# Performance work log

Hardware: AMD Instinct MI355X
Metric: run time of the kernel (lower is better)

Reference implementation:

```python
import jax, jax.numpy as jnp
import numpy as np
from jax.ops import segment_sum, segment_max

N = 100000   # nodes
E = 1600000  # edges
B = 256      # graphs
H = 128      # hidden_channels
F_IN = 4     # input_size
EPS = 1e-5


def _graph_norm(x, w, b, ms, batch):
    # PyG GraphNorm: out = w * (x - ms*mean_g) / sqrt(var_g + eps) + b
    cnt = jnp.maximum(segment_sum(jnp.ones((x.shape[0],), x.dtype), batch, num_segments=B), 1.0)
    mean = segment_sum(x, batch, num_segments=B) / cnt[:, None]
    out = x - mean[batch] * ms
    var = segment_sum(out * out, batch, num_segments=B) / cnt[:, None]
    return w * out / jnp.sqrt(var + EPS)[batch] + b


def _gcn(x, W, b, src, dst):
    # GCNConv with self-loops and symmetric normalization (src/dst already include self-loops)
    h = x @ W                                              # [N, H]
    deg = segment_sum(jnp.ones_like(src, dtype=h.dtype), dst, num_segments=N)
    dinv = jax.lax.rsqrt(jnp.maximum(deg, 1.0))
    norm = dinv[src] * dinv[dst]                           # [E+N]
    return segment_sum(norm[:, None] * h[src], dst, num_segments=N) + b


def _seg_softmax(gate, batch):
    gmax = segment_max(gate, batch, num_segments=B)
    e = jnp.exp(gate - gmax[batch])
    den = segment_sum(e, batch, num_segments=B)
    return e / den[batch]


def setup_inputs() -> dict:
    key = jax.random.key(0)
    ks = jax.random.split(key, 16)
    x = jax.random.normal(ks[0], (N, F_IN), jnp.float32)
    edge_index = jax.random.randint(ks[1], (2, E), 0, N, dtype=jnp.int64)
    batch = jnp.sort(jax.random.randint(ks[2], (N,), 0, B, dtype=jnp.int64))
    r = lambda k, shp, fan: jax.random.normal(k, shp, jnp.float32) / np.sqrt(fan)
    inp = {
        "x": x, "edge_index": edge_index, "batch": batch,
        "W1": r(ks[3], (F_IN, H), F_IN), "b1": jnp.zeros((H,), jnp.float32),
        "W2": r(ks[4], (H, H), H), "b2": jnp.zeros((H,), jnp.float32),
        "W3": r(ks[5], (H, H), H), "b3": jnp.zeros((H,), jnp.float32),
        "gn0_w": jnp.ones((F_IN,), jnp.float32), "gn0_b": jnp.zeros((F_IN,), jnp.float32), "gn0_ms": jnp.ones((F_IN,), jnp.float32),
        "gn1_w": jnp.ones((H,), jnp.float32), "gn1_b": jnp.zeros((H,), jnp.float32), "gn1_ms": jnp.ones((H,), jnp.float32),
        "gn2_w": jnp.ones((H,), jnp.float32), "gn2_b": jnp.zeros((H,), jnp.float32), "gn2_ms": jnp.ones((H,), jnp.float32),
        "gn3_w": jnp.ones((H,), jnp.float32), "gn3_b": jnp.zeros((H,), jnp.float32), "gn3_ms": jnp.ones((H,), jnp.float32),
        "g1": r(ks[6], (H, H), H), "gb1": jnp.zeros((H,), jnp.float32),
        "g2": r(ks[7], (H, H), H), "gb2": jnp.zeros((H,), jnp.float32),
        "g3": r(ks[8], (H, 1), H), "gb3": jnp.zeros((1,), jnp.float32),
        "l1": r(ks[9], (H, H), H), "lb1": jnp.zeros((H,), jnp.float32),
        "l2": r(ks[10], (H, H), H), "lb2": jnp.zeros((H,), jnp.float32),
        "l3": r(ks[11], (H, 1), H), "lb3": jnp.zeros((1,), jnp.float32),
    }
    return inp


def reference(x, edge_index, batch, W1, b1, W2, b2, W3, b3,
              gn0_w, gn0_b, gn0_ms, gn1_w, gn1_b, gn1_ms,
              gn2_w, gn2_b, gn2_ms, gn3_w, gn3_b, gn3_ms,
              g1, gb1, g2, gb2, g3, gb3,
              l1, lb1, l2, lb2, l3, lb3):
    loop = jnp.arange(N, dtype=edge_index.dtype)
    src = jnp.concatenate([edge_index[0], loop])
    dst = jnp.concatenate([edge_index[1], loop])

    h = _graph_norm(x, gn0_w, gn0_b, gn0_ms, batch)
    h = _gcn(h, W1, b1, src, dst)
    h = jax.nn.relu(_graph_norm(h, gn1_w, gn1_b, gn1_ms, batch))
    h = _gcn(h, W2, b2, src, dst)
    h = jax.nn.relu(_graph_norm(h, gn2_w, gn2_b, gn2_ms, batch))
    h = _gcn(h, W3, b3, src, dst)
    h = _graph_norm(h, gn3_w, gn3_b, gn3_ms, batch)

    # GlobalAttention: gate_nn -> scalar gate per node, segment softmax, weighted sum
    g = jax.nn.relu(h @ g1 + gb1)
    g = jax.nn.relu(g @ g2 + gb2)
    gate = g @ g3 + gb3                                   # [N, 1]
    attn = _seg_softmax(gate, batch)                      # [N, 1]
    pooled = segment_sum(attn * h, batch, num_segments=B) # [B, H]

    o = jax.nn.relu(pooled @ l1 + lb1)
    o = jax.nn.relu(o @ l2 + lb2)
    return o @ l3 + lb3                                   # [B, 1]
```

## Files before the change

kernel.cpp:

```cpp
#include <hip/hip_runtime.h>
#include <hip/hip_bf16.h>

#define NN 100000
#define NE 1600000
#define NB 256
#define HD 128
#define EPS 1e-5f
#define NBUK 1563
#define SLOTB 1536
#define EPB 8192
#define NCHK 8

typedef __attribute__((ext_vector_type(8))) short bf16x8v;
typedef __attribute__((ext_vector_type(4))) float f32x4v;

__device__ __forceinline__ float rd_dyn(const void* p, int i, int fflag) {
    if (fflag) {
        unsigned short u = ((const unsigned short*)p)[i];
        return __uint_as_float(((unsigned)u) << 16);
    }
    return ((const float*)p)[i];
}

__device__ __forceinline__ int rd_idx(const int* p, int k, int iflag) {
    return iflag ? p[k] : p[2 * k];
}

__device__ __forceinline__ unsigned short f2bf(float v) {
    __hip_bfloat16 b = __float2bfloat16(v);
    return *(unsigned short*)&b;
}

__device__ __forceinline__ float bflo(unsigned u) { return __uint_as_float(u << 16); }
__device__ __forceinline__ float bfhi(unsigned u) { return __uint_as_float(u & 0xFFFF0000u); }
__device__ __forceinline__ unsigned packbf(float a, float b) {
    return (unsigned)f2bf(a) | ((unsigned)f2bf(b) << 16);
}

__global__ void k_mark7(unsigned short* __restrict__ out, int n) {
    int i = blockIdx.x * blockDim.x + threadIdx.x;
    if (i < n) out[i] = 0x40E0;
}

__global__ void k_detect(const int* __restrict__ batch, const unsigned* __restrict__ w,
                         int* __restrict__ flags, int n) {
    int i = blockIdx.x * blockDim.x + threadIdx.x;
    if (i == 0 && w[0] == 0x3F803F80u) atomicOr(&flags[1], 1);
    if (i < n && (i & 1) && batch[i] != 0) atomicOr(&flags[0], 1);
}

struct CvtArgs {
    const void* p[30];
    int n[30];
    int off[30];
    const void* wp[4];
};
__global__ void k_cvtf_all(CvtArgs a, float* __restrict__ out,
                           unsigned short* __restrict__ WT,
                           const int* __restrict__ fflagp) {
    int j = blockIdx.y;
    int i = blockIdx.x * blockDim.x + threadIdx.x;
    int ff = *fflagp;
    if (j < 30) {
        if (i >= a.n[j]) return;
        out[a.off[j] + i] = rd_dyn(a.p[j], i, ff);
    } else {
        int mat = j - 30;
        if (i >= 16384) return;
        int nidx = i >> 7, k = i & 127;
        WT[mat * 16384 + nidx * 128 + k] = f2bf(rd_dyn(a.wp[mat], k * 128 + nidx, ff));
    }
}

__global__ void k_start(const int* __restrict__ batch, const int* __restrict__ iflagp,
                        int* __restrict__ start, int* __restrict__ batch32,
                        int* __restrict__ bcur, int n) {
    int i = blockIdx.x * blockDim.x + threadIdx.x;
    if (i >= n) return;
    if (i < NBUK) bcur[i] = i * SLOTB;
    int ifl = *iflagp;
    int b = rd_idx(batch, i, ifl); b = b < 0 ? 0 : (b > NB - 1 ? NB - 1 : b);
    batch32[i] = b;
    int bp;
    if (i == 0) bp = -1;
    else { bp = rd_idx(batch, i - 1, ifl); bp = bp < 0 ? 0 : (bp > NB - 1 ? NB - 1 : bp); }
    for (int g = bp + 1; g <= b; ++g) start[g] = i;
    if (i == n - 1) { for (int g = b + 1; g <= NB; ++g) start[g] = n; }
}

__global__ __launch_bounds__(256) void k_bfill(const int* __restrict__ ei,
                                               const int* __restrict__ iflagp,
                                               int* __restrict__ bcur,
                                               unsigned* __restrict__ bkte, int e) {
    __shared__ int lh[NBUK];
    __shared__ int lbase[NBUK];
    int ifl = *iflagp;
    for (int b = threadIdx.x; b < NBUK; b += 256) lh[b] = 0;
    __syncthreads();
    int s0 = blockIdx.x * EPB;
    int s1 = s0 + EPB; if (s1 > e) s1 = e;
    for (int i = s0 + threadIdx.x; i < s1; i += 256) {
        int d = rd_idx(ei, NE + i, ifl);
        int s = rd_idx(ei, i, ifl);
        if ((unsigned)d < (unsigned)NN && (unsigned)s < (unsigned)NN)
            atomicAdd(&lh[d >> 6], 1);
    }
    __syncthreads();
    for (int b = threadIdx.x; b < NBUK; b += 256) {
        int c = lh[b];
        if (c) { lbase[b] = atomicAdd(&bcur[b], c); lh[b] = 0; }
    }
    __syncthreads();
    for (int i = s0 + threadIdx.x; i < s1; i += 256) {
        int d = rd_idx(ei, NE + i, ifl);
        int s = rd_idx(ei, i, ifl);
        if ((unsigned)d < (unsigned)NN && (unsigned)s < (unsigned)NN) {
            int b = d >> 6;
            int li = atomicAdd(&lh[b], 1);
            bkte[lbase[b] + li] = ((unsigned)s << 6) | (unsigned)(d & 63);
        }
    }
}

__global__ __launch_bounds__(256) void k_csrfin(const unsigned* __restrict__ bkte,
                                                const int* __restrict__ bcur,
                                                int* __restrict__ rowptr,
                                                int* __restrict__ cnt,
                                                float* __restrict__ dinv,
                                                int* __restrict__ esrc) {
    __shared__ int lc[64];
    __shared__ int lcur[64];
    int b = blockIdx.x, t = threadIdx.x;
    int base = b * 64;
    if (t < 64) lc[t] = 0;
    __syncthreads();
    int r0 = b * SLOTB, r1 = bcur[b];
    for (int j = r0 + t; j < r1; j += 256)
        atomicAdd(&lc[(int)(bkte[j] & 63u)], 1);
    __syncthreads();
    if (t < 64) {
        int v = lc[t];
        int inc = v;
#pragma unroll
        for (int off = 1; off < 64; off <<= 1) {
            int nv = __shfl_up(inc, off, 64);
            if (t >= off) inc += nv;
        }
        int ex = r0 + inc - v;
        lcur[t] = ex;
        int node = base + t;
        if (node < NN) {
            rowptr[node] = ex;
            cnt[node] = v;
            dinv[node] = rsqrtf((float)(v + 1));
        }
    }
    __syncthreads();
    for (int j = r0 + t; j < r1; j += 256) {
        unsigned p = bkte[j];
        int slot = atomicAdd(&lcur[p & 63u], 1);
        esrc[slot] = (int)(p >> 6);
    }
}

__global__ __launch_bounds__(256) void k_gn4(const void* __restrict__ x,
                                             const float* __restrict__ w,
                                             const float* __restrict__ bb,
                                             const float* __restrict__ ms,
                                             const int* __restrict__ start,
                                             const int* __restrict__ fflagp,
                                             float* __restrict__ out) {
    int g = blockIdx.x;
    int s0 = start[g], s1 = start[g + 1];
    if (s1 <= s0) return;
    int ff = *fflagp;
    float cnt = (float)(s1 - s0);
    int t = threadIdx.x;
    __shared__ float4 rs[256], rq[256];
    float sx = 0.f, sy = 0.f, sz = 0.f, sw = 0.f;
    float qx = 0.f, qy = 0.f, qz = 0.f, qw = 0.f;
    for (int n = s0 + t; n < s1; n += 256) {
        float4 v;
        if (ff) {
            uint2 u = ((const uint2*)x)[n];
            v.x = bflo(u.x); v.y = bfhi(u.x); v.z = bflo(u.y); v.w = bfhi(u.y);
        } else {
            v = ((const float4*)x)[n];
        }
        sx += v.x; sy += v.y; sz += v.z; sw += v.w;
        qx = fmaf(v.x, v.x, qx); qy = fmaf(v.y, v.y, qy);
        qz = fmaf(v.z, v.z, qz); qw = fmaf(v.w, v.w, qw);
    }
    rs[t] = make_float4(sx, sy, sz, sw);
    rq[t] = make_float4(qx, qy, qz, qw);
    __syncthreads();
    for (int off = 128; off; off >>= 1) {
        if (t < off) {
            rs[t].x += rs[t + off].x; rs[t].y += rs[t + off].y;
            rs[t].z += rs[t + off].z; rs[t].w += rs[t + off].w;
            rq[t].x += rq[t + off].x; rq[t].y += rq[t + off].y;
            rq[t].z += rq[t + off].z; rq[t].w += rq[t + off].w;
        }
        __syncthreads();
    }
    float4 S = rs[0], Q = rq[0];
    float4 wv = ((const float4*)w)[0];
    float4 bv = ((const float4*)bb)[0];
    float4 mv = ((const float4*)ms)[0];
    float4 mean = make_float4(S.x / cnt, S.y / cnt, S.z / cnt, S.w / cnt);
    float4 sub = make_float4(mean.x * mv.x, mean.y * mv.y, mean.z * mv.z, mean.w * mv.w);
    float4 scale;
    scale.x = wv.x * rsqrtf(Q.x / cnt - 2.f * sub.x * mean.x + sub.x * sub.x + EPS);
    scale.y = wv.y * rsqrtf(Q.y / cnt - 2.f * sub.y * mean.y + sub.y * sub.y + EPS);
    scale.z = wv.z * rsqrtf(Q.z / cnt - 2.f * sub.z * mean.z + sub.z * sub.z + EPS);
    scale.w = wv.w * rsqrtf(Q.w / cnt - 2.f * sub.w * mean.w + sub.w * sub.w + EPS);
    float4* op = (float4*)out;
    for (int n = s0 + t; n < s1; n += 256) {
        float4 v;
        if (ff) {
            uint2 u = ((const uint2*)x)[n];
            v.x = bflo(u.x); v.y = bfhi(u.x); v.z = bflo(u.y); v.w = bfhi(u.y);
        } else {
            v = ((const float4*)x)[n];
        }
        float4 o;
        o.x = scale.x * (v.x - sub.x) + bv.x;
        o.y = scale.y * (v.y - sub.y) + bv.y;
        o.z = scale.z * (v.z - sub.z) + bv.z;
        o.w = scale.w * (v.w - sub.w) + bv.w;
        op[n] = o;
    }
}

__global__ __launch_bounds__(256) void k_gnstats_part(const unsigned* __restrict__ Xu,
                                                      const int* __restrict__ start,
                                                      float* __restrict__ PS,
                                                      float* __restrict__ PQ) {
    int g = blockIdx.x, k = blockIdx.y;
    int s0 = start[g], s1 = start[g + 1];
    int len = (s1 - s0 + NCHK - 1) / NCHK;
    int c0 = s0 + k * len, c1 = c0 + len; if (c1 > s1) c1 = s1;
    int t = threadIdx.x;
    int cp = t & 63, p = t >> 6;
    __shared__ float r0s[256], r1s[256], r0q[256], r1q[256];
    float s0a = 0.f, s1a = 0.f, q0a = 0.f, q1a = 0.f;
    for (int n = c0 + p; n < c1; n += 4) {
        unsigned u = Xu[n * 64 + cp];
        float lo = bflo(u), hi = bfhi(u);
        s0a += lo; q0a = fmaf(lo, lo, q0a);
        s1a += hi; q1a = fmaf(hi, hi, q1a);
    }
    r0s[t] = s0a; r1s[t] = s1a; r0q[t] = q0a; r1q[t] = q1a;
    __syncthreads();
    if (p == 0) {
        float a0 = r0s[cp] + r0s[64 + cp] + r0s[128 + cp] + r0s[192 + cp];
        float a1 = r1s[cp] + r1s[64 + cp] + r1s[128 + cp] + r1s[192 + cp];
        float b0 = r0q[cp] + r0q[64 + cp] + r0q[128 + cp] + r0q[192 + cp];
        float b1 = r1q[cp] + r1q[64 + cp] + r1q[128 + cp] + r1q[192 + cp];
        int bidx = (g * NCHK + k) * 128;
        PS[bidx + 2 * cp] = a0; PS[bidx + 2 * cp + 1] = a1;
        PQ[bidx + 2 * cp] = b0; PQ[bidx + 2 * cp + 1] = b1;
    }
}

__global__ __launch_bounds__(128) void k_gnstats_final(const float* __restrict__ PS,
                                                       const float* __restrict__ PQ,
                                                       const float* __restrict__ w,
                                                       const float* __restrict__ ms,
                                                       const int* __restrict__ start,
                                                       float* __restrict__ SUB,
                                                       float* __restrict__ SCALE) {
    int g = blockIdx.x, c = threadIdx.x;
    int n = start[g + 1] - start[g];
    if (n <= 0) return;
    float cnt = (float)n;
    float s = 0.f, q = 0.f;
#pragma unroll
    for (int k = 0; k < NCHK; ++k) {
        s += PS[(g * NCHK + k) * 128 + c];
        q += PQ[(g * NCHK + k) * 128 + c];
    }
    float mean = s / cnt;
    float sq = q / cnt;
    float sub = mean * ms[c];
    float var = sq - 2.f * sub * mean + sub * sub;
    SUB[g * 128 + c] = sub;
    SCALE[g * 128 + c] = w[c] * rsqrtf(var + EPS);
}

__global__ __launch_bounds__(256) void k_gather4gemm(const int* __restrict__ rowptr,
                                                     const int* __restrict__ cnt,
                                                     const int* __restrict__ esrc,
                                                     const float* __restrict__ dinv,
                                                     const float* __restrict__ h0,
                                                     const float* __restrict__ W1,
                                                     const float* __restrict__ b1,
                                                     unsigned* __restrict__ Xu) {
    __shared__ float w1s[512];
    __shared__ float b1s[128];
    int tid = threadIdx.x;
    w1s[tid] = W1[tid];
    w1s[256 + tid] = W1[256 + tid];
    if (tid < 128) b1s[tid] = b1[tid];
    __syncthreads();
    int node = blockIdx.x * 4 + (tid >> 6);
    int lane = tid & 63;
    if (node >= NN) return;
    int r0 = rowptr[node], r1 = r0 + cnt[node];
    const float4* h4 = (const float4*)h0;
    float ax = 0.f, ay = 0.f, az = 0.f, aw = 0.f;
    for (int j = r0 + lane; j < r1; j += 64) {
        int s = esrc[j];
        float dv = dinv[s];
        float4 h = h4[s];
        ax = fmaf(dv, h.x, ax); ay = fmaf(dv, h.y, ay);
        az = fmaf(dv, h.z, az); aw = fmaf(dv, h.w, aw);
    }
#pragma unroll
    for (int mask = 1; mask <= 32; mask <<= 1) {
        ax += __shfl_xor(ax, mask, 64); ay += __shfl_xor(ay, mask, 64);
        az += __shfl_xor(az, mask, 64); aw += __shfl_xor(aw, mask, 64);
    }
    float dd = dinv[node];
    float4 hn = h4[node];
    float za = dd * ax + dd * dd * hn.x;
    float zb = dd * ay + dd * dd * hn.y;
    float zc = dd * az + dd * dd * hn.z;
    float zd = dd * aw + dd * dd * hn.w;
    int c0 = 2 * lane, c1 = 2 * lane + 1;
    float v0 = za * w1s[c0] + zb * w1s[128 + c0] + zc * w1s[256 + c0] + zd * w1s[384 + c0] + b1s[c0];
    float v1 = za * w1s[c1] + zb * w1s[128 + c1] + zc * w1s[256 + c1] + zd * w1s[384 + c1] + b1s[c1];
    Xu[node * 64 + lane] = packbf(v0, v1);
}

__global__ __launch_bounds__(256) void k_gemm_mfma_bf(const unsigned* __restrict__ Xu,
                                                      const int* __restrict__ batch32,
                                                      const float* __restrict__ SUB,
                                                      const float* __restrict__ SCALE,
                                                      const float* __restrict__ gnb,
                                                      int relu,
                                                      const unsigned short* __restrict__ WT,
                                                      const float* __restrict__ dinv,
                                                      unsigned short* __restrict__ out) {
    __shared__ unsigned short xs[16][136];
    int base = blockIdx.x * 16;
    int tid = threadIdx.x;
    for (int idx = tid; idx < 1024; idx += 256) {
        int r = idx >> 6, cp = idx & 63;
        int g = batch32[base + r];
        unsigned u = Xu[(base + r) * 64 + cp];
        float2 sub = ((const float2*)(SUB + g * 128))[cp];
        float2 sc  = ((const float2*)(SCALE + g * 128))[cp];
        float2 gb  = ((const float2*)gnb)[cp];
        float va = (bflo(u) - sub.x) * sc.x + gb.x;
        float vb = (bfhi(u) - sub.y) * sc.y + gb.y;
        if (relu) { va = fmaxf(va, 0.f); vb = fmaxf(vb, 0.f); }
        xs[r][2 * cp] = f2bf(va);
        xs[r][2 * cp + 1] = f2bf(vb);
    }
    __syncthreads();
    int wave = tid >> 6, lane = tid & 63;
    int m = lane & 15, quad = lane >> 4;
    f32x4v acc0 = {0.f, 0.f, 0.f, 0.f}, acc1 = {0.f, 0.f, 0.f, 0.f};
    int c0 = wave * 32 + m, c1 = c0 + 16;
#pragma unroll
    for (int kk = 0; kk < 4; ++kk) {
        int ko = kk * 32 + quad * 8;
        bf16x8v a  = *(const bf16x8v*)&xs[m][ko];
        bf16x8v b0 = *(const bf16x8v*)&WT[c0 * 128 + ko];
        bf16x8v b1 = *(const bf16x8v*)&WT[c1 * 128 + ko];
        acc0 = __builtin_amdgcn_mfma_f32_16x16x32_bf16(a, b0, acc0, 0, 0, 0);
        acc1 = __builtin_amdgcn_mfma_f32_16x16x32_bf16(a, b1, acc1, 0, 0, 0);
    }
#pragma unroll
    for (int reg = 0; reg < 4; ++reg) {
        int row = base + quad * 4 + reg;
        float dv = dinv[row];
        out[row * 128 + c0] = f2bf(dv * acc0[reg]);
        out[row * 128 + c1] = f2bf(dv * acc1[reg]);
    }
}

#define ACC4(u) do { \
    a0 += bflo((u).x); a1 += bfhi((u).x); \
    a2 += bflo((u).y); a3 += bfhi((u).y); \
    a4 += bflo((u).z); a5 += bfhi((u).z); \
    a6 += bflo((u).w); a7 += bfhi((u).w); } while (0)

__global__ __launch_bounds__(256) void k_gather_bf(const int* __restrict__ rowptr,
                                                   const int* __restrict__ cnt,
                                                   const int* __restrict__ esrc,
                                                   const float* __restrict__ dinv,
                                                   const unsigned* __restrict__ h,
                                                   const float* __restrict__ bias,
                                                   unsigned* __restrict__ Xu) {
    int node = blockIdx.x * 4 + (threadIdx.x >> 6);
    int lane = threadIdx.x & 63;
    if (node >= NN) return;
    int q = lane >> 4, s = lane & 15;
    int r0 = rowptr[node], r1 = r0 + cnt[node];
    const uint4* hp = (const uint4*)h;
    float a0 = 0.f, a1 = 0.f, a2 = 0.f, a3 = 0.f;
    float a4 = 0.f, a5 = 0.f, a6 = 0.f, a7 = 0.f;
    int j = r0 + q;
    for (; j + 12 < r1; j += 16) {
        int e0 = esrc[j], e1 = esrc[j + 4], e2 = esrc[j + 8], e3 = esrc[j + 12];
        uint4 u0 = hp[e0 * 16 + s];
        uint4 u1 = hp[e1 * 16 + s];
        uint4 u2 = hp[e2 * 16 + s];
        uint4 u3 = hp[e3 * 16 + s];
        ACC4(u0); ACC4(u1); ACC4(u2); ACC4(u3);
    }
    for (; j + 4 < r1; j += 8) {
        int e0 = esrc[j], e1 = esrc[j + 4];
        uint4 u0 = hp[e0 * 16 + s];
        uint4 u1 = hp[e1 * 16 + s];
        ACC4(u0); ACC4(u1);
    }
    for (; j < r1; j += 4) {
        int e0 = esrc[j];
        uint4 u0 = hp[e0 * 16 + s];
        ACC4(u0);
    }
    a0 += __shfl_xor(a0, 16, 64); a0 += __shfl_xor(a0, 32, 64);
    a1 += __shfl_xor(a1, 16, 64); a1 += __shfl_xor(a1, 32, 64);
    a2 += __shfl_xor(a2, 16, 64); a2 += __shfl_xor(a2, 32, 64);
    a3 += __shfl_xor(a3, 16, 64); a3 += __shfl_xor(a3, 32, 64);
    a4 += __shfl_xor(a4, 16, 64); a4 += __shfl_xor(a4, 32, 64);
    a5 += __shfl_xor(a5, 16, 64); a5 += __shfl_xor(a5, 32, 64);
    a6 += __shfl_xor(a6, 16, 64); a6 += __shfl_xor(a6, 32, 64);
    a7 += __shfl_xor(a7, 16, 64); a7 += __shfl_xor(a7, 32, 64);
    int cp = 4 * s + q;
    float ax = q == 0 ? a0 : q == 1 ? a2 : q == 2 ? a4 : a6;
    float ay = q == 0 ? a1 : q == 1 ? a3 : q == 2 ? a5 : a7;
    float dd = dinv[node];
    unsigned us = h[node * 64 + cp];
    float2 bb = ((const float2*)bias)[cp];
    float ox = dd * (ax + bflo(us)) + bb.x;
    float oy = dd * (ay + bfhi(us)) + bb.y;
    Xu[node * 64 + cp] = packbf(ox, oy);
}

__global__ __launch_bounds__(256) void k_gate_fused(const unsigned* __restrict__ Xu,
                                                    const int* __restrict__ batch32,
                                                    const float* __restrict__ SUB,
                                                    const float* __restrict__ SCALE,
                                                    const float* __restrict__ gnb,
                                                    const unsigned short* __restrict__ GT1,
                                                    const float* __restrict__ gb1,
                                                    const unsigned short* __restrict__ GT2,
                                                    const float* __restrict__ gb2,
                                                    const float* __restrict__ g3,
                                                    const float* __restrict__ gb3,
                                                    float* __restrict__ gate) {
    __shared__ unsigned short xs[16][136];
    __shared__ unsigned short t1[16][136];
    __shared__ float redw[64];
    int base = blockIdx.x * 16;
    int tid = threadIdx.x;
    for (int idx = tid; idx < 1024; idx += 256) {
        int r = idx >> 6, cp = idx & 63;
        int g = batch32[base + r];
        unsigned u = Xu[(base + r) * 64 + cp];
        float2 sub = ((const float2*)(SUB + g * 128))[cp];
        float2 sc  = ((const float2*)(SCALE + g * 128))[cp];
        float2 gb  = ((const float2*)gnb)[cp];
        xs[r][2 * cp] = f2bf((bflo(u) - sub.x) * sc.x + gb.x);
        xs[r][2 * cp + 1] = f2bf((bfhi(u) - sub.y) * sc.y + gb.y);
    }
    __syncthreads();
    int wave = tid >> 6, lane = tid & 63;
    int m = lane & 15, quad = lane >> 4;
    int c0 = wave * 32 + m, c1 = c0 + 16;
    f32x4v acc0 = {0.f, 0.f, 0.f, 0.f}, acc1 = {0.f, 0.f, 0.f, 0.f};
#pragma unroll
    for (int kk = 0; kk < 4; ++kk) {
        int ko = kk * 32 + quad * 8;
        bf16x8v a  = *(const bf16x8v*)&xs[m][ko];
        bf16x8v b0 = *(const bf16x8v*)&GT1[c0 * 128 + ko];
        bf16x8v b1 = *(const bf16x8v*)&GT1[c1 * 128 + ko];
        acc0 = __builtin_amdgcn_mfma_f32_16x16x32_bf16(a, b0, acc0, 0, 0, 0);
        acc1 = __builtin_amdgcn_mfma_f32_16x16x32_bf16(a, b1, acc1, 0, 0, 0);
    }
    float bj0 = gb1[c0], bj1 = gb1[c1];
#pragma unroll
    for (int reg = 0; reg < 4; ++reg) {
        int row = quad * 4 + reg;
        t1[row][c0] = f2bf(fmaxf(acc0[reg] + bj0, 0.f));
        t1[row][c1] = f2bf(fmaxf(acc1[reg] + bj1, 0.f));
    }
    __syncthreads();
    f32x4v d0 = {0.f, 0.f, 0.f, 0.f}, d1 = {0.f, 0.f, 0.f, 0.f};
#pragma unroll
    for (int kk = 0; kk < 4; ++kk) {
        int ko = kk * 32 + quad * 8;
        bf16x8v a  = *(const bf16x8v*)&t1[m][ko];
        bf16x8v b0 = *(const bf16x8v*)&GT2[c0 * 128 + ko];
        bf16x8v b1 = *(const bf16x8v*)&GT2[c1 * 128 + ko];
        d0 = __builtin_amdgcn_mfma_f32_16x16x32_bf16(a, b0, d0, 0, 0, 0);
        d1 = __builtin_amdgcn_mfma_f32_16x16x32_bf16(a, b1, d1, 0, 0, 0);
    }
    float g30 = g3[c0], g31 = g3[c1];
    float bk0 = gb2[c0], bk1 = gb2[c1];
    float contrib[4];
#pragma unroll
    for (int reg = 0; reg < 4; ++reg) {
        float v0 = fmaxf(d0[reg] + bk0, 0.f);
        float v1 = fmaxf(d1[reg] + bk1, 0.f);
        contrib[reg] = v0 * g30 + v1 * g31;
    }
#pragma unroll
    for (int mask = 1; mask <= 8; mask <<= 1) {
#pragma unroll
        for (int reg = 0; reg < 4; ++reg)
            contrib[reg] += __shfl_xor(contrib[reg], mask, 64);
    }
    if (m == 0) {
#pragma unroll
        for (int reg = 0; reg < 4; ++reg)
            redw[wave * 16 + quad * 4 + reg] = contrib[reg];
    }
    __syncthreads();
    if (tid < 16) {
        float s = redw[tid] + redw[16 + tid] + redw[32 + tid] + redw[48 + tid];
        gate[base + tid] = s + gb3[0];
    }
}

__global__ __launch_bounds__(256) void k_smpool(const unsigned* __restrict__ Xu,
                                                const float* __restrict__ SUB,
                                                const float* __restrict__ SCALE,
                                                const float* __restrict__ gnb,
                                                const float* __restrict__ gate,
                                                const int* __restrict__ start,
                                                float* __restrict__ PP) {
    int g = blockIdx.x, kk = blockIdx.y;
    int s0 = start[g], s1 = start[g + 1];
    int t = threadIdx.x;
    __shared__ float red[256];
    __shared__ float r0s[256], r1s[256];
    if (s1 <= s0) {
        if (t < 64) {
            int bidx = (g * NCHK + kk) * 128;
            ((float2*)(PP + bidx))[t] = make_float2(0.f, 0.f);
        }
        return;
    }
    float m = -1e30f;
    for (int i = s0 + t; i < s1; i += 256) m = fmaxf(m, gate[i]);
    red[t] = m; __syncthreads();
    for (int off = 128; off; off >>= 1) { if (t < off) red[t] = fmaxf(red[t], red[t + off]); __syncthreads(); }
    m = red[0]; __syncthreads();
    float sden = 0.f;
    for (int i = s0 + t; i < s1; i += 256) sden += expf(gate[i] - m);
    red[t] = sden; __syncthreads();
    for (int off = 128; off; off >>= 1) { if (t < off) red[t] += red[t + off]; __syncthreads(); }
    float invden = 1.f / red[0];
    int len = (s1 - s0 + NCHK - 1) / NCHK;
    int c0 = s0 + kk * len, c1 = c0 + len; if (c1 > s1) c1 = s1;
    int cp = t & 63, p = t >> 6;
    float2 sub = ((const float2*)(SUB + g * 128))[cp];
    float2 sc  = ((const float2*)(SCALE + g * 128))[cp];
    float2 gb  = ((const float2*)gnb)[cp];
    float sa = 0.f, sb = 0.f;
    for (int n = c0 + p; n < c1; n += 4) {
        float a = expf(gate[n] - m) * invden;
        unsigned u = Xu[n * 64 + cp];
        sa += a * ((bflo(u) - sub.x) * sc.x + gb.x);
        sb += a * ((bfhi(u) - sub.y) * sc.y + gb.y);
    }
    r0s[t] = sa; r1s[t] = sb; __syncthreads();
    if (p == 0) {
        int bidx = (g * NCHK + kk) * 128;
        float2 o;
        o.x = r0s[cp] + r0s[64 + cp] + r0s[128 + cp] + r0s[192 + cp];
        o.y = r1s[cp] + r1s[64 + cp] + r1s[128 + cp] + r1s[192 + cp];
        ((float2*)(PP + bidx))[cp] = o;
    }
}

__global__ __launch_bounds__(128) void k_head(const float* __restrict__ PP,
                                              const float* __restrict__ l1, const float* __restrict__ lb1,
                                              const float* __restrict__ l2, const float* __restrict__ lb2,
                                              const float* __restrict__ l3, const float* __restrict__ lb3,
                                              const int* __restrict__ fflagp,
                                              void* __restrict__ out) {
    int g = blockIdx.x, t = threadIdx.x;
    __shared__ float p[128], o[128], red[128];
    float s = 0.f;
#pragma unroll
    for (int k = 0; k < NCHK; ++k) s += PP[(g * NCHK + k) * 128 + t];
    p[t] = s; __syncthreads();
    float a = 0.f;
    for (int k = 0; k < 128; ++k) a += p[k] * l1[k * 128 + t];
    a = fmaxf(a + lb1[t], 0.f);
    o[t] = a; __syncthreads();
    float b = 0.f;
    for (int k = 0; k < 128; ++k) b += o[k] * l2[k * 128 + t];
    b = fmaxf(b + lb2[t], 0.f);
    red[t] = b * l3[t]; __syncthreads();
    for (int off = 64; off; off >>= 1) { if (t < off) red[t] += red[t + off]; __syncthreads(); }
    if (t == 0) {
        float r = red[0] + lb3[0];
        if (*fflagp) ((__hip_bfloat16*)out)[g] = __float2bfloat16(r);
        else ((float*)out)[g] = r;
    }
}

extern "C" void kernel_launch(void* const* d_in, const int* in_sizes, int n_in,
                              void* d_out, int out_size, void* d_ws, size_t ws_size,
                              hipStream_t stream) {
    const void* x = d_in[0];
    const int* ei_raw = (const int*)d_in[1];
    const int* batch_raw = (const int*)d_in[2];
    (void)n_in; (void)out_size;

    char* ws = (char*)d_ws;
    size_t off = 0;
    auto alloc = [&](size_t bytes) -> void* {
        void* p = ws + off;
        off += (bytes + 255) & ~(size_t)255;
        return p;
    };
    unsigned* Xu  = (unsigned*)alloc((size_t)NN * HD * 2);
    float* Y      = (float*)alloc((size_t)NN * HD * 4);
    float* h0     = (float*)alloc((size_t)NN * 4 * 4);
    float* dinv   = (float*)alloc((size_t)NN * 4);
    float* gate   = (float*)alloc((size_t)NN * 4);
    int*   start  = (int*)alloc((size_t)(NB + 1) * 4);
    int*   batch32= (int*)alloc((size_t)NN * 4);
    float* P      = (float*)alloc((size_t)131072 * 4);
    unsigned short* WT = (unsigned short*)alloc((size_t)4 * 16384 * 2);
    float* SUB    = (float*)alloc((size_t)NB * HD * 4);
    float* SCALE  = (float*)alloc((size_t)NB * HD * 4);
    float* PS     = (float*)alloc((size_t)NB * NCHK * 128 * 4);
    float* PQ     = (float*)alloc((size_t)NB * NCHK * 128 * 4);
    int*   flags  = (int*)alloc(256);
    int*   rowptr = (int*)alloc((size_t)NN * 4);
    int*   cnt    = (int*)alloc((size_t)NN * 4);
    int*   esrc   = (int*)alloc((size_t)NBUK * SLOTB * 4);
    int*   bcur   = (int*)alloc((size_t)NBUK * 4);
    unsigned* bkte = (unsigned*)(Y + (size_t)NN * HD / 2);
    float* PP = PS;

    if (ws_size < off) {
        k_mark7<<<1, 256, 0, stream>>>((unsigned short*)d_out, NB);
        return;
    }

    int* iflag = flags;
    int* fflag = flags + 1;
    hipMemsetAsync(flags, 0, 8, stream);
    k_detect<<<(NN + 255) / 256, 256, 0, stream>>>(batch_raw, (const unsigned*)d_in[12], flags, NN);

    CvtArgs ca;
    float* fp[33];
    int maxn = 16384;
    {
        int poff = 0;
        for (int i = 3; i < 33; ++i) {
            int n = in_sizes[i];
            ca.p[i - 3] = d_in[i];
            ca.n[i - 3] = n;
            ca.off[i - 3] = poff;
            fp[i] = P + poff;
            poff += n;
            if (n > maxn) maxn = n;
        }
        ca.wp[0] = d_in[5];
        ca.wp[1] = d_in[7];
        ca.wp[2] = d_in[21];
        ca.wp[3] = d_in[23];
    }
    {
        dim3 grid((maxn + 255) / 256, 34);
        k_cvtf_all<<<grid, 256, 0, stream>>>(ca, P, WT, fflag);
    }
    const float *W1 = fp[3], *b1 = fp[4], *b2 = fp[6], *b3 = fp[8];
    const float *gn0w = fp[9],  *gn0b = fp[10], *gn0m = fp[11];
    const float *gn1w = fp[12], *gn1b = fp[13], *gn1m = fp[14];
    const float *gn2w = fp[15], *gn2b = fp[16], *gn2m = fp[17];
    const float *gn3w = fp[18], *gn3b = fp[19], *gn3m = fp[20];
    const float *gb1 = fp[22], *gb2 = fp[24], *g3 = fp[25], *gb3 = fp[26];
    const float *l1 = fp[27], *lb1 = fp[28], *l2 = fp[29], *lb2 = fp[30], *l3 = fp[31], *lb3 = fp[32];

    const unsigned short* WT2 = WT;
    const unsigned short* WT3 = WT + 16384;
    const unsigned short* GT1 = WT + 2 * 16384;
    const unsigned short* GT2 = WT + 3 * 16384;

    k_start<<<(NN + 255) / 256, 256, 0, stream>>>(batch_raw, iflag, start, batch32, bcur, NN);

    int ebg = (NE + EPB - 1) / EPB;
    k_bfill<<<ebg, 256, 0, stream>>>(ei_raw, iflag, bcur, bkte, NE);
    k_csrfin<<<NBUK, 256, 0, stream>>>(bkte, bcur, rowptr, cnt, dinv, esrc);

    k_gn4<<<NB, 256, 0, stream>>>(x, gn0w, gn0b, gn0m, start, fflag, h0);

    k_gather4gemm<<<(NN + 3) / 4, 256, 0, stream>>>(rowptr, cnt, esrc, dinv, h0, W1, b1, Xu);

    unsigned short* Yb = (unsigned short*)Y;
    dim3 sgrid(NB, NCHK);

    k_gnstats_part<<<sgrid, 256, 0, stream>>>(Xu, start, PS, PQ);
    k_gnstats_final<<<NB, 128, 0, stream>>>(PS, PQ, gn1w, gn1m, start, SUB, SCALE);
    k_gemm_mfma_bf<<<NN / 16, 256, 0, stream>>>(Xu, batch32, SUB, SCALE, gn1b, 1, WT2, dinv, Yb);
    k_gather_bf<<<(NN + 3) / 4, 256, 0, stream>>>(rowptr, cnt, esrc, dinv, (const unsigned*)Yb, b2, Xu);

    k_gnstats_part<<<sgrid, 256, 0, stream>>>(Xu, start, PS, PQ);
    k_gnstats_final<<<NB, 128, 0, stream>>>(PS, PQ, gn2w, gn2m, start, SUB, SCALE);
    k_gemm_mfma_bf<<<NN / 16, 256, 0, stream>>>(Xu, batch32, SUB, SCALE, gn2b, 1, WT3, dinv, Yb);
    k_gather_bf<<<(NN + 3) / 4, 256, 0, stream>>>(rowptr, cnt, esrc, dinv, (const unsigned*)Yb, b3, Xu);

    k_gnstats_part<<<sgrid, 256, 0, stream>>>(Xu, start, PS, PQ);
    k_gnstats_final<<<NB, 128, 0, stream>>>(PS, PQ, gn3w, gn3m, start, SUB, SCALE);
    k_gate_fused<<<NN / 16, 256, 0, stream>>>(Xu, batch32, SUB, SCALE, gn3b,
                                              GT1, gb1, GT2, gb2, g3, gb3, gate);
    k_smpool<<<sgrid, 256, 0, stream>>>(Xu, SUB, SCALE, gn3b, gate, start, PP);
    k_head<<<NB, 128, 0, stream>>>(PP, l1, lb1, l2, lb2, l3, lb3, fflag, d_out);
}
```

Measured before the change: 532.7 us.

## Fuse prep, CSR finalize with GraphNorm0, stats and pooling-head kernels

Merges k_start into the conversion kernel and k_csrfin with the first GraphNorm in one launch. Replaces the two-stage GraphNorm stats (partials plus final) with a single kernel per graph and channel segment. Merges softmax pooling with the MLP head, caching attention weights in shared memory. It also changes the first gather to spread channels across lanes. The aim is fewer launches and intermediate buffers, at the cost of less parallelism per graph in the stats and pooling kernels (256 or 1024 blocks instead of 2048).

```diff
diff --git a/kernel.cpp b/kernel.cpp
--- a/kernel.cpp
+++ b/kernel.cpp
@@ -9,7 +9,7 @@
 #define NBUK 1563
 #define SLOTB 1536
 #define EPB 8192
-#define NCHK 8
+#define MAXG 768
 
 typedef __attribute__((ext_vector_type(8))) short bf16x8v;
 typedef __attribute__((ext_vector_type(4))) float f32x4v;
@@ -55,37 +55,34 @@
     int off[30];
     const void* wp[4];
 };
-__global__ void k_cvtf_all(CvtArgs a, float* __restrict__ out,
-                           unsigned short* __restrict__ WT,
-                           const int* __restrict__ fflagp) {
+__global__ void k_prep(CvtArgs a, float* __restrict__ out,
+                       unsigned short* __restrict__ WT,
+                       const int* __restrict__ flagsp,
+                       const int* __restrict__ batch,
+                       int* __restrict__ start, int* __restrict__ batch32,
+                       int* __restrict__ bcur) {
     int j = blockIdx.y;
     int i = blockIdx.x * blockDim.x + threadIdx.x;
-    int ff = *fflagp;
     if (j < 30) {
         if (i >= a.n[j]) return;
-        out[a.off[j] + i] = rd_dyn(a.p[j], i, ff);
-    } else {
+        out[a.off[j] + i] = rd_dyn(a.p[j], i, flagsp[1]);
+    } else if (j < 34) {
         int mat = j - 30;
         if (i >= 16384) return;
         int nidx = i >> 7, k = i & 127;
-        WT[mat * 16384 + nidx * 128 + k] = f2bf(rd_dyn(a.wp[mat], k * 128 + nidx, ff));
-    }
-}
-
-__global__ void k_start(const int* __restrict__ batch, const int* __restrict__ iflagp,
-                        int* __restrict__ start, int* __restrict__ batch32,
-                        int* __restrict__ bcur, int n) {
-    int i = blockIdx.x * blockDim.x + threadIdx.x;
-    if (i >= n) return;
-    if (i < NBUK) bcur[i] = i * SLOTB;
-    int ifl = *iflagp;
-    int b = rd_idx(batch, i, ifl); b = b < 0 ? 0 : (b > NB - 1 ? NB - 1 : b);
-    batch32[i] = b;
-    int bp;
-    if (i == 0) bp = -1;
-    else { bp = rd_idx(batch, i - 1, ifl); bp = bp < 0 ? 0 : (bp > NB - 1 ? NB - 1 : bp); }
-    for (int g = bp + 1; g <= b; ++g) start[g] = i;
-    if (i == n - 1) { for (int g = b + 1; g <= NB; ++g) start[g] = n; }
+        WT[mat * 16384 + nidx * 128 + k] = f2bf(rd_dyn(a.wp[mat], k * 128 + nidx, flagsp[1]));
+    } else {
+        if (i >= NN) return;
+        if (i < NBUK) bcur[i] = i * SLOTB;
+        int ifl = flagsp[0];
+        int b = rd_idx(batch, i, ifl); b = b < 0 ? 0 : (b > NB - 1 ? NB - 1 : b);
+        batch32[i] = b;
+        int bp;
+        if (i == 0) bp = -1;
+        else { bp = rd_idx(batch, i - 1, ifl); bp = bp < 0 ? 0 : (bp > NB - 1 ? NB - 1 : bp); }
+        for (int g = bp + 1; g <= b; ++g) start[g] = i;
+        if (i == NN - 1) { for (int g = b + 1; g <= NB; ++g) start[g] = NN; }
+    }
 }
 
 __global__ __launch_bounds__(256) void k_bfill(const int* __restrict__ ei,
@@ -122,61 +119,62 @@
     }
 }
 
-__global__ __launch_bounds__(256) void k_csrfin(const unsigned* __restrict__ bkte,
-                                                const int* __restrict__ bcur,
-                                                int* __restrict__ rowptr,
-                                                int* __restrict__ cnt,
-                                                float* __restrict__ dinv,
-                                                int* __restrict__ esrc) {
-    __shared__ int lc[64];
-    __shared__ int lcur[64];
-    int b = blockIdx.x, t = threadIdx.x;
-    int base = b * 64;
-    if (t < 64) lc[t] = 0;
-    __syncthreads();
-    int r0 = b * SLOTB, r1 = bcur[b];
-    for (int j = r0 + t; j < r1; j += 256)
-        atomicAdd(&lc[(int)(bkte[j] & 63u)], 1);
-    __syncthreads();
-    if (t < 64) {
-        int v = lc[t];
-        int inc = v;
-#pragma unroll
-        for (int off = 1; off < 64; off <<= 1) {
-            int nv = __shfl_up(inc, off, 64);
-            if (t >= off) inc += nv;
-        }
-        int ex = r0 + inc - v;
-        lcur[t] = ex;
-        int node = base + t;
-        if (node < NN) {
-            rowptr[node] = ex;
-            cnt[node] = v;
-            dinv[node] = rsqrtf((float)(v + 1));
-        }
-    }
-    __syncthreads();
-    for (int j = r0 + t; j < r1; j += 256) {
-        unsigned p = bkte[j];
-        int slot = atomicAdd(&lcur[p & 63u], 1);
-        esrc[slot] = (int)(p >> 6);
-    }
-}
-
-__global__ __launch_bounds__(256) void k_gn4(const void* __restrict__ x,
-                                             const float* __restrict__ w,
-                                             const float* __restrict__ bb,
-                                             const float* __restrict__ ms,
-                                             const int* __restrict__ start,
-                                             const int* __restrict__ fflagp,
-                                             float* __restrict__ out) {
-    int g = blockIdx.x;
+__global__ __launch_bounds__(256) void k_csrfin_gn4(const unsigned* __restrict__ bkte,
+                                                    const int* __restrict__ bcur,
+                                                    int* __restrict__ rowptr,
+                                                    int* __restrict__ cnt,
+                                                    float* __restrict__ dinv,
+                                                    int* __restrict__ esrc,
+                                                    const void* __restrict__ x,
+                                                    const float* __restrict__ w,
+                                                    const float* __restrict__ bb,
+                                                    const float* __restrict__ ms,
+                                                    const int* __restrict__ start,
+                                                    const int* __restrict__ fflagp,
+                                                    float* __restrict__ out) {
+    int t = threadIdx.x;
+    if (blockIdx.x < NBUK) {
+        __shared__ int lc[64];
+        __shared__ int lcur[64];
+        int b = blockIdx.x;
+        int base = b * 64;
+        if (t < 64) lc[t] = 0;
+        __syncthreads();
+        int r0 = b * SLOTB, r1 = bcur[b];
+        for (int j = r0 + t; j < r1; j += 256)
+            atomicAdd(&lc[(int)(bkte[j] & 63u)], 1);
+        __syncthreads();
+        if (t < 64) {
+            int v = lc[t];
+            int inc = v;
+#pragma unroll
+            for (int off = 1; off < 64; off <<= 1) {
+                int nv = __shfl_up(inc, off, 64);
+                if (t >= off) inc += nv;
+            }
+            int ex = r0 + inc - v;
+            lcur[t] = ex;
+            int node = base + t;
+            if (node < NN) {
+                rowptr[node] = ex;
+                cnt[node] = v;
+                dinv[node] = rsqrtf((float)(v + 1));
+            }
+        }
+        __syncthreads();
+        for (int j = r0 + t; j < r1; j += 256) {
+            unsigned p = bkte[j];
+            int slot = atomicAdd(&lcur[p & 63u], 1);
+            esrc[slot] = (int)(p >> 6);
+        }
+        return;
+    }
+    __shared__ float4 rs[256], rq[256];
+    int g = blockIdx.x - NBUK;
     int s0 = start[g], s1 = start[g + 1];
     if (s1 <= s0) return;
     int ff = *fflagp;
-    float cnt = (float)(s1 - s0);
-    int t = threadIdx.x;
-    __shared__ float4 rs[256], rq[256];
+    float cntf = (float)(s1 - s0);
     float sx = 0.f, sy = 0.f, sz = 0.f, sw = 0.f;
     float qx = 0.f, qy = 0.f, qz = 0.f, qw = 0.f;
     for (int n = s0 + t; n < s1; n += 256) {
@@ -207,13 +205,13 @@
     float4 wv = ((const float4*)w)[0];
     float4 bv = ((const float4*)bb)[0];
     float4 mv = ((const float4*)ms)[0];
-    float4 mean = make_float4(S.x / cnt, S.y / cnt, S.z / cnt, S.w / cnt);
+    float4 mean = make_float4(S.x / cntf, S.y / cntf, S.z / cntf, S.w / cntf);
     float4 sub = make_float4(mean.x * mv.x, mean.y * mv.y, mean.z * mv.z, mean.w * mv.w);
     float4 scale;
-    scale.x = wv.x * rsqrtf(Q.x / cnt - 2.f * sub.x * mean.x + sub.x * sub.x + EPS);
-    scale.y = wv.y * rsqrtf(Q.y / cnt - 2.f * sub.y * mean.y + sub.y * sub.y + EPS);
-    scale.z = wv.z * rsqrtf(Q.z / cnt - 2.f * sub.z * mean.z + sub.z * sub.z + EPS);
-    scale.w = wv.w * rsqrtf(Q.w / cnt - 2.f * sub.w * mean.w + sub.w * sub.w + EPS);
+    scale.x = wv.x * rsqrtf(Q.x / cntf - 2.f * sub.x * mean.x + sub.x * sub.x + EPS);
+    scale.y = wv.y * rsqrtf(Q.y / cntf - 2.f * sub.y * mean.y + sub.y * sub.y + EPS);
+    scale.z = wv.z * rsqrtf(Q.z / cntf - 2.f * sub.z * mean.z + sub.z * sub.z + EPS);
+    scale.w = wv.w * rsqrtf(Q.w / cntf - 2.f * sub.w * mean.w + sub.w * sub.w + EPS);
     float4* op = (float4*)out;
     for (int n = s0 + t; n < s1; n += 256) {
         float4 v;
@@ -232,60 +230,47 @@
     }
 }
 
-__global__ __launch_bounds__(256) void k_gnstats_part(const unsigned* __restrict__ Xu,
-                                                      const int* __restrict__ start,
-                                                      float* __restrict__ PS,
-                                                      float* __restrict__ PQ) {
-    int g = blockIdx.x, k = blockIdx.y;
+__global__ __launch_bounds__(256) void k_gnstats1(const unsigned* __restrict__ Xu,
+                                                  const float* __restrict__ w,
+                                                  const float* __restrict__ ms,
+                                                  const int* __restrict__ start,
+                                                  float* __restrict__ SUB,
+                                                  float* __restrict__ SCALE) {
+    int g = blockIdx.x, seg = blockIdx.y;
     int s0 = start[g], s1 = start[g + 1];
-    int len = (s1 - s0 + NCHK - 1) / NCHK;
-    int c0 = s0 + k * len, c1 = c0 + len; if (c1 > s1) c1 = s1;
+    if (s1 <= s0) return;
     int t = threadIdx.x;
-    int cp = t & 63, p = t >> 6;
-    __shared__ float r0s[256], r1s[256], r0q[256], r1q[256];
-    float s0a = 0.f, s1a = 0.f, q0a = 0.f, q1a = 0.f;
-    for (int n = c0 + p; n < c1; n += 4) {
-        unsigned u = Xu[n * 64 + cp];
+    int wrd = t & 15;
+    int p = t >> 4;
+    int wbase = seg * 16 + wrd;
+    __shared__ float rs0[256], rs1[256], rq0[256], rq1[256];
+    float sa = 0.f, sb = 0.f, qa = 0.f, qb = 0.f;
+    for (int n = s0 + p; n < s1; n += 16) {
+        unsigned u = Xu[(size_t)n * 64 + wbase];
         float lo = bflo(u), hi = bfhi(u);
-        s0a += lo; q0a = fmaf(lo, lo, q0a);
-        s1a += hi; q1a = fmaf(hi, hi, q1a);
-    }
-    r0s[t] = s0a; r1s[t] = s1a; r0q[t] = q0a; r1q[t] = q1a;
-    __syncthreads();
-    if (p == 0) {
-        float a0 = r0s[cp] + r0s[64 + cp] + r0s[128 + cp] + r0s[192 + cp];
-        float a1 = r1s[cp] + r1s[64 + cp] + r1s[128 + cp] + r1s[192 + cp];
-        float b0 = r0q[cp] + r0q[64 + cp] + r0q[128 + cp] + r0q[192 + cp];
-        float b1 = r1q[cp] + r1q[64 + cp] + r1q[128 + cp] + r1q[192 + cp];
-        int bidx = (g * NCHK + k) * 128;
-        PS[bidx + 2 * cp] = a0; PS[bidx + 2 * cp + 1] = a1;
-        PQ[bidx + 2 * cp] = b0; PQ[bidx + 2 * cp + 1] = b1;
-    }
-}
-
-__global__ __launch_bounds__(128) void k_gnstats_final(const float* __restrict__ PS,
-                                                       const float* __restrict__ PQ,
-                                                       const float* __restrict__ w,
-                                                       const float* __restrict__ ms,
-                                                       const int* __restrict__ start,
-                                                       float* __restrict__ SUB,
-                                                       float* __restrict__ SCALE) {
-    int g = blockIdx.x, c = threadIdx.x;
-    int n = start[g + 1] - start[g];
-    if (n <= 0) return;
-    float cnt = (float)n;
-    float s = 0.f, q = 0.f;
-#pragma unroll
-    for (int k = 0; k < NCHK; ++k) {
-        s += PS[(g * NCHK + k) * 128 + c];
-        q += PQ[(g * NCHK + k) * 128 + c];
-    }
-    float mean = s / cnt;
-    float sq = q / cnt;
-    float sub = mean * ms[c];
-    float var = sq - 2.f * sub * mean + sub * sub;
-    SUB[g * 128 + c] = sub;
-    SCALE[g * 128 + c] = w[c] * rsqrtf(var + EPS);
+        sa += lo; qa = fmaf(lo, lo, qa);
+        sb += hi; qb = fmaf(hi, hi, qb);
+    }
+    rs0[t] = sa; rs1[t] = sb; rq0[t] = qa; rq1[t] = qb;
+    __syncthreads();
+    for (int off = 128; off >= 16; off >>= 1) {
+        if (t < off) {
+            rs0[t] += rs0[t + off]; rs1[t] += rs1[t + off];
+            rq0[t] += rq0[t + off]; rq1[t] += rq1[t + off];
+        }
+        __syncthreads();
+    }
+    if (t < 16) {
+        float cnt = (float)(s1 - s0);
+        int c0 = 2 * (seg * 16 + t), c1 = c0 + 1;
+        float mean0 = rs0[t] / cnt, mean1 = rs1[t] / cnt;
+        float sub0 = mean0 * ms[c0], sub1 = mean1 * ms[c1];
+        float var0 = rq0[t] / cnt - 2.f * sub0 * mean0 + sub0 * sub0;
+        float var1 = rq1[t] / cnt - 2.f * sub1 * mean1 + sub1 * sub1;
+        SUB[g * 128 + c0] = sub0; SUB[g * 128 + c1] = sub1;
+        SCALE[g * 128 + c0] = w[c0] * rsqrtf(var0 + EPS);
+        SCALE[g * 128 + c1] = w[c1] * rsqrtf(var1 + EPS);
+    }
 }
 
 __global__ __launch_bounds__(256) void k_gather4gemm(const int* __restrict__ rowptr,
@@ -306,27 +291,20 @@
     int node = blockIdx.x * 4 + (tid >> 6);
     int lane = tid & 63;
     if (node >= NN) return;
+    int ch = lane & 3;
     int r0 = rowptr[node], r1 = r0 + cnt[node];
-    const float4* h4 = (const float4*)h0;
-    float ax = 0.f, ay = 0.f, az = 0.f, aw = 0.f;
-    for (int j = r0 + lane; j < r1; j += 64) {
+    float acc = 0.f;
+    for (int j = r0 + (lane >> 2); j < r1; j += 16) {
         int s = esrc[j];
-        float dv = dinv[s];
-        float4 h = h4[s];
-        ax = fmaf(dv, h.x, ax); ay = fmaf(dv, h.y, ay);
-        az = fmaf(dv, h.z, az); aw = fmaf(dv, h.w, aw);
-    }
-#pragma unroll
-    for (int mask = 1; mask <= 32; mask <<= 1) {
-        ax += __shfl_xor(ax, mask, 64); ay += __shfl_xor(ay, mask, 64);
-        az += __shfl_xor(az, mask, 64); aw += __shfl_xor(aw, mask, 64);
-    }
+        acc = fmaf(dinv[s], h0[s * 4 + ch], acc);
+    }
+#pragma unroll
+    for (int mask = 4; mask <= 32; mask <<= 1)
+        acc += __shfl_xor(acc, mask, 64);
     float dd = dinv[node];
-    float4 hn = h4[node];
-    float za = dd * ax + dd * dd * hn.x;
-    float zb = dd * ay + dd * dd * hn.y;
-    float zc = dd * az + dd * dd * hn.z;
-    float zd = dd * aw + dd * dd * hn.w;
+    float z = dd * acc + dd * dd * h0[node * 4 + ch];
+    float za = __shfl(z, 0, 64), zb = __shfl(z, 1, 64);
+    float zc = __shfl(z, 2, 64), zd = __shfl(z, 3, 64);
     int c0 = 2 * lane, c1 = 2 * lane + 1;
     float v0 = za * w1s[c0] + zb * w1s[128 + c0] + zc * w1s[256 + c0] + zd * w1s[384 + c0] + b1s[c0];
     float v1 = za * w1s[c1] + zb * w1s[128 + c1] + zc * w1s[256 + c1] + zd * w1s[384 + c1] + b1s[c1];
@@ -527,78 +505,86 @@
     }
 }
 
-__global__ __launch_bounds__(256) void k_smpool(const unsigned* __restrict__ Xu,
-                                                const float* __restrict__ SUB,
-                                                const float* __restrict__ SCALE,
-                                                const float* __restrict__ gnb,
-                                                const float* __restrict__ gate,
-                                                const int* __restrict__ start,
-                                                float* __restrict__ PP) {
-    int g = blockIdx.x, kk = blockIdx.y;
+__global__ __launch_bounds__(256) void k_smpool_head(const unsigned* __restrict__ Xu,
+                                                     const float* __restrict__ SUB,
+                                                     const float* __restrict__ SCALE,
+                                                     const float* __restrict__ gnb,
+                                                     const float* __restrict__ gate,
+                                                     const int* __restrict__ start,
+                                                     const float* __restrict__ l1, const float* __restrict__ lb1,
+                                                     const float* __restrict__ l2, const float* __restrict__ lb2,
+                                                     const float* __restrict__ l3, const float* __restrict__ lb3,
+                                                     const int* __restrict__ fflagp,
+                                                     void* __restrict__ out) {
+    int g = blockIdx.x, t = threadIdx.x;
+    __shared__ float red[256];
+    __shared__ float att[MAXG];
+    __shared__ float4 rs4[256];
+    __shared__ float pool[128];
+    __shared__ float o[128];
     int s0 = start[g], s1 = start[g + 1];
-    int t = threadIdx.x;
-    __shared__ float red[256];
-    __shared__ float r0s[256], r1s[256];
-    if (s1 <= s0) {
-        if (t < 64) {
-            int bidx = (g * NCHK + kk) * 128;
-            ((float2*)(PP + bidx))[t] = make_float2(0.f, 0.f);
-        }
-        return;
-    }
+    int len = s1 - s0;
+    bool fits = len <= MAXG;
     float m = -1e30f;
     for (int i = s0 + t; i < s1; i += 256) m = fmaxf(m, gate[i]);
     red[t] = m; __syncthreads();
     for (int off = 128; off; off >>= 1) { if (t < off) red[t] = fmaxf(red[t], red[t + off]); __syncthreads(); }
     m = red[0]; __syncthreads();
     float sden = 0.f;
-    for (int i = s0 + t; i < s1; i += 256) sden += expf(gate[i] - m);
+    for (int i = s0 + t; i < s1; i += 256) {
+        float e = expf(gate[i] - m);
+        if (fits) att[i - s0] = e;
+        sden += e;
+    }
     red[t] = sden; __syncthreads();
     for (int off = 128; off; off >>= 1) { if (t < off) red[t] += red[t + off]; __syncthreads(); }
-    float invden = 1.f / red[0];
-    int len = (s1 - s0 + NCHK - 1) / NCHK;
-    int c0 = s0 + kk * len, c1 = c0 + len; if (c1 > s1) c1 = s1;
-    int cp = t & 63, p = t >> 6;
-    float2 sub = ((const float2*)(SUB + g * 128))[cp];
-    float2 sc  = ((const float2*)(SCALE + g * 128))[cp];
-    float2 gb  = ((const float2*)gnb)[cp];
-    float sa = 0.f, sb = 0.f;
-    for (int n = c0 + p; n < c1; n += 4) {
-        float a = expf(gate[n] - m) * invden;
-        unsigned u = Xu[n * 64 + cp];
-        sa += a * ((bflo(u) - sub.x) * sc.x + gb.x);
-        sb += a * ((bfhi(u) - sub.y) * sc.y + gb.y);
-    }
-    r0s[t] = sa; r1s[t] = sb; __syncthreads();
-    if (p == 0) {
-        int bidx = (g * NCHK + kk) * 128;
-        float2 o;
-        o.x = r0s[cp] + r0s[64 + cp] + r0s[128 + cp] + r0s[192 + cp];
-        o.y = r1s[cp] + r1s[64 + cp] + r1s[128 + cp] + r1s[192 + cp];
-        ((float2*)(PP + bidx))[cp] = o;
-    }
-}
-
-__global__ __launch_bounds__(128) void k_head(const float* __restrict__ PP,
-                                              const float* __restrict__ l1, const float* __restrict__ lb1,
-                                              const float* __restrict__ l2, const float* __restrict__ lb2,
-                                              const float* __restrict__ l3, const float* __restrict__ lb3,
-                                              const int* __restrict__ fflagp,
-                                              void* __restrict__ out) {
-    int g = blockIdx.x, t = threadIdx.x;
-    __shared__ float p[128], o[128], red[128];
-    float s = 0.f;
-#pragma unroll
-    for (int k = 0; k < NCHK; ++k) s += PP[(g * NCHK + k) * 128 + t];
-    p[t] = s; __syncthreads();
-    float a = 0.f;
-    for (int k = 0; k < 128; ++k) a += p[k] * l1[k * 128 + t];
-    a = fmaxf(a + lb1[t], 0.f);
-    o[t] = a; __syncthreads();
-    float b = 0.f;
-    for (int k = 0; k < 128; ++k) b += o[k] * l2[k * 128 + t];
-    b = fmaxf(b + lb2[t], 0.f);
-    red[t] = b * l3[t]; __syncthreads();
+    float invden = len > 0 ? 1.f / red[0] : 0.f;
+    __syncthreads();
+    int cp2 = t & 31, p = t >> 5;
+    float4 sb4 = {0.f, 0.f, 0.f, 0.f}, sc4 = {0.f, 0.f, 0.f, 0.f}, gb4 = {0.f, 0.f, 0.f, 0.f};
+    if (len > 0) {
+        sb4 = ((const float4*)(SUB + g * 128))[cp2];
+        sc4 = ((const float4*)(SCALE + g * 128))[cp2];
+        gb4 = ((const float4*)gnb)[cp2];
+    }
+    float a0 = 0.f, a1 = 0.f, a2 = 0.f, a3 = 0.f;
+    for (int n = s0 + p; n < s1; n += 8) {
+        float a = (fits ? att[n - s0] : expf(gate[n] - m)) * invden;
+        uint2 u = ((const uint2*)(Xu + (size_t)n * 64))[cp2];
+        a0 += a * ((bflo(u.x) - sb4.x) * sc4.x + gb4.x);
+        a1 += a * ((bfhi(u.x) - sb4.y) * sc4.y + gb4.y);
+        a2 += a * ((bflo(u.y) - sb4.z) * sc4.z + gb4.z);
+        a3 += a * ((bfhi(u.y) - sb4.w) * sc4.w + gb4.w);
+    }
+    rs4[t] = make_float4(a0, a1, a2, a3);
+    __syncthreads();
+    for (int off = 128; off >= 32; off >>= 1) {
+        if (t < off) {
+            rs4[t].x += rs4[t + off].x; rs4[t].y += rs4[t + off].y;
+            rs4[t].z += rs4[t + off].z; rs4[t].w += rs4[t + off].w;
+        }
+        __syncthreads();
+    }
+    if (t < 32) {
+        pool[4 * t]     = rs4[t].x;
+        pool[4 * t + 1] = rs4[t].y;
+        pool[4 * t + 2] = rs4[t].z;
+        pool[4 * t + 3] = rs4[t].w;
+    }
+    __syncthreads();
+    if (t < 128) {
+        float a = 0.f;
+        for (int k = 0; k < 128; ++k) a += pool[k] * l1[k * 128 + t];
+        o[t] = fmaxf(a + lb1[t], 0.f);
+    }
+    __syncthreads();
+    if (t < 128) {
+        float b = 0.f;
+        for (int k = 0; k < 128; ++k) b += o[k] * l2[k * 128 + t];
+        b = fmaxf(b + lb2[t], 0.f);
+        red[t] = b * l3[t];
+    }
+    __syncthreads();
     for (int off = 64; off; off >>= 1) { if (t < off) red[t] += red[t + off]; __syncthreads(); }
     if (t == 0) {
         float r = red[0] + lb3[0];
@@ -633,15 +619,12 @@
     unsigned short* WT = (unsigned short*)alloc((size_t)4 * 16384 * 2);
     float* SUB    = (float*)alloc((size_t)NB * HD * 4);
     float* SCALE  = (float*)alloc((size_t)NB * HD * 4);
-    float* PS     = (float*)alloc((size_t)NB * NCHK * 128 * 4);
-    float* PQ     = (float*)alloc((size_t)NB * NCHK * 128 * 4);
     int*   flags  = (int*)alloc(256);
     int*   rowptr = (int*)alloc((size_t)NN * 4);
     int*   cnt    = (int*)alloc((size_t)NN * 4);
     int*   esrc   = (int*)alloc((size_t)NBUK * SLOTB * 4);
     int*   bcur   = (int*)alloc((size_t)NBUK * 4);
     unsigned* bkte = (unsigned*)(Y + (size_t)NN * HD / 2);
-    float* PP = PS;
 
     if (ws_size < off) {
         k_mark7<<<1, 256, 0, stream>>>((unsigned short*)d_out, NB);
@@ -655,7 +638,6 @@
 
     CvtArgs ca;
     float* fp[33];
-    int maxn = 16384;
     {
         int poff = 0;
         for (int i = 3; i < 33; ++i) {
@@ -665,7 +647,6 @@
             ca.off[i - 3] = poff;
             fp[i] = P + poff;
             poff += n;
-            if (n > maxn) maxn = n;
         }
         ca.wp[0] = d_in[5];
         ca.wp[1] = d_in[7];
@@ -673,12 +654,12 @@
         ca.wp[3] = d_in[23];
     }
     {
-        dim3 grid((maxn + 255) / 256, 34);
-        k_cvtf_all<<<grid, 256, 0, stream>>>(ca, P, WT, fflag);
+        dim3 grid((NN + 255) / 256, 35);
+        k_prep<<<grid, 256, 0, stream>>>(ca, P, WT, flags, batch_raw, start, batch32, bcur);
     }
     const float *W1 = fp[3], *b1 = fp[4], *b2 = fp[6], *b3 = fp[8];
     const float *gn0w = fp[9],  *gn0b = fp[10], *gn0m = fp[11];
-    const float *gn1w = fp[12], *gn1b = fp[13], *gn1m = fp[14];
+    const float *gn1w = fp[12], *gn1m = fp[14], *gn1b = fp[13];
     const float *gn2w = fp[15], *gn2b = fp[16], *gn2m = fp[17];
     const float *gn3w = fp[18], *gn3b = fp[19], *gn3m = fp[20];
     const float *gb1 = fp[22], *gb2 = fp[24], *g3 = fp[25], *gb3 = fp[26];
@@ -689,33 +670,27 @@
     const unsigned short* GT1 = WT + 2 * 16384;
     const unsigned short* GT2 = WT + 3 * 16384;
 
-    k_start<<<(NN + 255) / 256, 256, 0, stream>>>(batch_raw, iflag, start, batch32, bcur, NN);
-
     int ebg = (NE + EPB - 1) / EPB;
     k_bfill<<<ebg, 256, 0, stream>>>(ei_raw, iflag, bcur, bkte, NE);
-    k_csrfin<<<NBUK, 256, 0, stream>>>(bkte, bcur, rowptr, cnt, dinv, esrc);
-
-    k_gn4<<<NB, 256, 0, stream>>>(x, gn0w, gn0b, gn0m, start, fflag, h0);
+    k_csrfin_gn4<<<NBUK + NB, 256, 0, stream>>>(bkte, bcur, rowptr, cnt, dinv, esrc,
+                                                x, gn0w, gn0b, gn0m, start, fflag, h0);
 
     k_gather4gemm<<<(NN + 3) / 4, 256, 0, stream>>>(rowptr, cnt, esrc, dinv, h0, W1, b1, Xu);
 
     unsigned short* Yb = (unsigned short*)Y;
-    dim3 sgrid(NB, NCHK);
-
-    k_gnstats_part<<<sgrid, 256, 0, stream>>>(Xu, start, PS, PQ);
-    k_gnstats_final<<<NB, 128, 0, stream>>>(PS, PQ, gn1w, gn1m, start, SUB, SCALE);
+    dim3 sgrid(NB, 4);
+
+    k_gnstats1<<<sgrid, 256, 0, stream>>>(Xu, gn1w, gn1m, start, SUB, SCALE);
     k_gemm_mfma_bf<<<NN / 16, 256, 0, stream>>>(Xu, batch32, SUB, SCALE, gn1b, 1, WT2, dinv, Yb);
     k_gather_bf<<<(NN + 3) / 4, 256, 0, stream>>>(rowptr, cnt, esrc, dinv, (const unsigned*)Yb, b2, Xu);
 
-    k_gnstats_part<<<sgrid, 256, 0, stream>>>(Xu, start, PS, PQ);
-    k_gnstats_final<<<NB, 128, 0, stream>>>(PS, PQ, gn2w, gn2m, start, SUB, SCALE);
+    k_gnstats1<<<sgrid, 256, 0, stream>>>(Xu, gn2w, gn2m, start, SUB, SCALE);
     k_gemm_mfma_bf<<<NN / 16, 256, 0, stream>>>(Xu, batch32, SUB, SCALE, gn2b, 1, WT3, dinv, Yb);
     k_gather_bf<<<(NN + 3) / 4, 256, 0, stream>>>(rowptr, cnt, esrc, dinv, (const unsigned*)Yb, b3, Xu);
 
-    k_gnstats_part<<<sgrid, 256, 0, stream>>>(Xu, start, PS, PQ);
-    k_gnstats_final<<<NB, 128, 0, stream>>>(PS, PQ, gn3w, gn3m, start, SUB, SCALE);
+    k_gnstats1<<<sgrid, 256, 0, stream>>>(Xu, gn3w, gn3m, start, SUB, SCALE);
     k_gate_fused<<<NN / 16, 256, 0, stream>>>(Xu, batch32, SUB, SCALE, gn3b,
                                               GT1, gb1, GT2, gb2, g3, gb3, gate);
-    k_smpool<<<sgrid, 256, 0, stream>>>(Xu, SUB, SCALE, gn3b, gate, start, PP);
-    k_head<<<NB, 128, 0, stream>>>(PP, l1, lb1, l2, lb2, l3, lb3, fflag, d_out);
-}
+    k_smpool_head<<<NB, 256, 0, stream>>>(Xu, SUB, SCALE, gn3b, gate, start,
+                                          l1, lb1, l2, lb2, l3, lb3, fflag, d_out);
+}
```

Measured after the change: 539.4 us. Within noise of the previous version (+1.2%).
